# Optimization experiments

Measured on AMD Instinct MI355X. Metric: run time of the kernel, lower is better.

## Reference

```python
import jax, jax.numpy as jnp
import numpy as np
from jax.scipy.special import gammaln

RES = 512    # init res
STEPS = 128  # init steps


def setup_inputs() -> dict:
    key = jax.random.key(0)
    # control points in [0,1]^2: [batch, n_strks, n_points, 2]
    control_points = jax.random.uniform(key, (16, 4, 4, 2), dtype=jnp.float32)
    sigma = jnp.float32(0.02)  # Gaussian kernel bandwidth
    return {"control_points": control_points, "sigma": sigma}


def _bernstein(order, n_steps):
    # feat[k, t] = C(order, k) * t**(order-k) * (1-t)**k, matching sample_curve
    t = jnp.linspace(0.0, 1.0, n_steps, dtype=jnp.float32)          # [T]
    k = jnp.arange(order + 1, dtype=jnp.float32)[:, None]           # [K,1]
    o = jnp.float32(order)
    log_comb = gammaln(o + 1.0) - gammaln(k + 1.0) - gammaln(o - k + 1.0)
    return jnp.exp(log_comb) * t[None, :] ** (o - k) * (1.0 - t[None, :]) ** k  # [K,T]


def reference(control_points, sigma):
    """Bezier.forward with method='base', keep_strk_dim=True.
    Returns [batch, n_strks, 1, res, res]."""
    b, s, n_pts, _ = control_points.shape
    feat = _bernstein(n_pts - 1, STEPS)                              # [K,T]
    curve = jnp.einsum('bcki,kt->bcit', control_points, feat)       # [b,s,2,T]
    x = curve[:, :, 0]                                               # [b,s,T]
    y = curve[:, :, 1]                                               # [b,s,T]
    g = jnp.arange(RES, dtype=jnp.float32) / RES                     # pixel coords
    inv = 1.0 / (2.0 * sigma ** 2)
    # Gaussian splat is separable: exp(-(dx^2+dy^2)/2s^2) = exp(-dx^2/2s^2)*exp(-dy^2/2s^2)
    # raster[b,s,p,q] = sum_t Ay[b,s,t,p] * Ax[b,s,t,q]  (x indexes columns q, y rows p,
    # matching torch meshgrid + transpose(1,3) layout)
    Ax = jnp.exp(-(x[..., None] - g) ** 2 * inv)                     # [b,s,T,res]
    Ay = jnp.exp(-(y[..., None] - g) ** 2 * inv)                     # [b,s,T,res]
    raster = jnp.einsum('bstp,bstq->bspq', Ay, Ax)                   # [b,s,res,res]
    return raster[:, :, None]                                        # [b,s,1,res,res]
```

## Files before the change

kernel.cpp:

```cpp
#include <hip/hip_runtime.h>
#include <math.h>

#define RES    512
#define STEPS  128
#define BH     16
#define NCHUNK 8

__global__ __launch_bounds__(256) void bezier_band_kernel(
    const float* __restrict__ cp,
    const float* __restrict__ sigma_ptr,
    float* __restrict__ out)
{
    __shared__ float xb[STEPS];
    __shared__ float yb[STEPS];
    __shared__ float ayc[STEPS][BH];
    __shared__ unsigned char clist[NCHUNK][STEPS];
    __shared__ int  ccnt[NCHUNK];
    __shared__ int  nb_s;

    const int img  = blockIdx.y;
    const int p0   = blockIdx.x * BH;
    const int tid  = threadIdx.x;
    const int lane = tid & 63;
    const int wave = tid >> 6;

    const float sigma  = sigma_ptr[0];
    const float inv    = 1.0f / (2.0f * sigma * sigma);
    const float msq    = 16.0f / inv;
    const float margin = sqrtf(msq);

    if (tid == 0) nb_s = 0;
    __syncthreads();

    if (tid < STEPS) {
        const float w  = (float)tid * (1.0f / 127.0f);
        const float v  = 1.0f - w;
        const float b0 = w * w * w;
        const float b1 = 3.0f * w * w * v;
        const float b2 = 3.0f * w * v * v;
        const float b3 = v * v * v;
        const float* c = cp + (size_t)img * 8;
        const float x = c[0]*b0 + c[2]*b1 + c[4]*b2 + c[6]*b3;
        const float y = c[1]*b0 + c[3]*b1 + c[5]*b2 + c[7]*b3;
        const float lo = (float)p0            * (1.0f / RES) - margin;
        const float hi = (float)(p0 + BH - 1) * (1.0f / RES) + margin;
        if (y >= lo && y <= hi) {
            const int s = atomicAdd(&nb_s, 1);
            xb[s] = x;
            yb[s] = y;
        }
    }
    __syncthreads();
    const int nb = nb_s;

    for (int e = tid; e < nb * BH; e += 256) {
        const int s = e >> 4;
        const int i = e & (BH - 1);
        const float dy = yb[s] - (float)(p0 + i) * (1.0f / RES);
        ayc[s][i] = __expf(-dy * dy * inv);
    }

    #pragma unroll
    for (int cc = 0; cc < 2; ++cc) {
        const int c = wave + 4 * cc;
        const float lo = (float)(c * 64)      * (1.0f / RES) - margin;
        const float hi = (float)(c * 64 + 63) * (1.0f / RES) + margin;
        int cnt = 0;
        for (int base = 0; base < nb; base += 64) {
            const int s = base + lane;
            const bool act = (s < nb) && (xb[s] >= lo) && (xb[s] <= hi);
            const unsigned long long m = __ballot(act);
            if (act) {
                const int pos = __popcll(m & ((1ull << lane) - 1ull));
                clist[c][cnt + pos] = (unsigned char)s;
            }
            cnt += __popcll(m);
        }
        if (lane == 0) ccnt[c] = cnt;
    }
    __syncthreads();

    float acc0[BH], acc1[BH];
    #pragma unroll
    for (int i = 0; i < BH; ++i) { acc0[i] = 0.0f; acc1[i] = 0.0f; }

    const float gq0 = (float)tid         * (1.0f / RES);
    const float gq1 = (float)(tid + 256) * (1.0f / RES);
    const int c0 = wave;
    const int c1 = wave + 4;

    const int n0 = ccnt[c0];
    for (int j = 0; j < n0; ++j) {
        const int   s  = clist[c0][j];
        const float dx = xb[s] - gq0;
        const float ax = __expf(-dx * dx * inv);
        const float4 a0 = *(const float4*)&ayc[s][0];
        const float4 a1 = *(const float4*)&ayc[s][4];
        const float4 a2 = *(const float4*)&ayc[s][8];
        const float4 a3 = *(const float4*)&ayc[s][12];
        acc0[0]  += ax * a0.x; acc0[1]  += ax * a0.y;
        acc0[2]  += ax * a0.z; acc0[3]  += ax * a0.w;
        acc0[4]  += ax * a1.x; acc0[5]  += ax * a1.y;
        acc0[6]  += ax * a1.z; acc0[7]  += ax * a1.w;
        acc0[8]  += ax * a2.x; acc0[9]  += ax * a2.y;
        acc0[10] += ax * a2.z; acc0[11] += ax * a2.w;
        acc0[12] += ax * a3.x; acc0[13] += ax * a3.y;
        acc0[14] += ax * a3.z; acc0[15] += ax * a3.w;
    }
    const int n1 = ccnt[c1];
    for (int j = 0; j < n1; ++j) {
        const int   s  = clist[c1][j];
        const float dx = xb[s] - gq1;
        const float ax = __expf(-dx * dx * inv);
        const float4 a0 = *(const float4*)&ayc[s][0];
        const float4 a1 = *(const float4*)&ayc[s][4];
        const float4 a2 = *(const float4*)&ayc[s][8];
        const float4 a3 = *(const float4*)&ayc[s][12];
        acc1[0]  += ax * a0.x; acc1[1]  += ax * a0.y;
        acc1[2]  += ax * a0.z; acc1[3]  += ax * a0.w;
        acc1[4]  += ax * a1.x; acc1[5]  += ax * a1.y;
        acc1[6]  += ax * a1.z; acc1[7]  += ax * a1.w;
        acc1[8]  += ax * a2.x; acc1[9]  += ax * a2.y;
        acc1[10] += ax * a2.z; acc1[11] += ax * a2.w;
        acc1[12] += ax * a3.x; acc1[13] += ax * a3.y;
        acc1[14] += ax * a3.z; acc1[15] += ax * a3.w;
    }

    #pragma unroll
    for (int i = 0; i < BH; ++i) {
        const size_t rowoff = ((size_t)img * RES + (size_t)(p0 + i)) * RES;
        out[rowoff + tid]       = acc0[i];
        out[rowoff + tid + 256] = acc1[i];
    }
}

extern "C" void kernel_launch(void* const* d_in, const int* in_sizes, int n_in,
                              void* d_out, int out_size, void* d_ws, size_t ws_size,
                              hipStream_t stream) {
    const float* cp    = (const float*)d_in[0];
    const float* sigma = (const float*)d_in[1];
    float* out         = (float*)d_out;
    const int n_img    = in_sizes[0] / 8;
    dim3 grid(RES / BH, n_img);
    bezier_band_kernel<<<grid, 256, 0, stream>>>(cp, sigma, out);
}
```

Measured before the change: 92.42 us.

## Use 512-thread blocks, one column chunk per wave, with image-interleaved block order

Blocks grow from 256 to 512 threads, so each wave handles a single 64-column chunk with one 16-row accumulator set instead of two sequential chunks. This halves per-thread serial work and register pressure. The grid is flattened with the image index in the low bits so neighbouring blocks cover different images, which spreads load across compute units. The hit loop is also unrolled by two. The hard-coded `& 63` assumes exactly 64 images and breaks for any other batch size.

```diff
diff --git a/kernel.cpp b/kernel.cpp
--- a/kernel.cpp
+++ b/kernel.cpp
@@ -6,7 +6,7 @@
 #define BH     16
 #define NCHUNK 8
 
-__global__ __launch_bounds__(256) void bezier_band_kernel(
+__global__ __launch_bounds__(512) void bezier_band_kernel(
     const float* __restrict__ cp,
     const float* __restrict__ sigma_ptr,
     float* __restrict__ out)
@@ -18,8 +18,9 @@
     __shared__ int  ccnt[NCHUNK];
     __shared__ int  nb_s;
 
-    const int img  = blockIdx.y;
-    const int p0   = blockIdx.x * BH;
+    const int bid  = blockIdx.x;
+    const int img  = bid & 63;
+    const int p0   = (bid >> 6) * BH;
     const int tid  = threadIdx.x;
     const int lane = tid & 63;
     const int wave = tid >> 6;
@@ -53,18 +54,16 @@
     __syncthreads();
     const int nb = nb_s;
 
-    for (int e = tid; e < nb * BH; e += 256) {
+    for (int e = tid; e < nb * BH; e += 512) {
         const int s = e >> 4;
         const int i = e & (BH - 1);
         const float dy = yb[s] - (float)(p0 + i) * (1.0f / RES);
         ayc[s][i] = __expf(-dy * dy * inv);
     }
 
-    #pragma unroll
-    for (int cc = 0; cc < 2; ++cc) {
-        const int c = wave + 4 * cc;
-        const float lo = (float)(c * 64)      * (1.0f / RES) - margin;
-        const float hi = (float)(c * 64 + 63) * (1.0f / RES) + margin;
+    {
+        const float lo = (float)(wave * 64)      * (1.0f / RES) - margin;
+        const float hi = (float)(wave * 64 + 63) * (1.0f / RES) + margin;
         int cnt = 0;
         for (int base = 0; base < nb; base += 64) {
             const int s = base + lane;
@@ -72,65 +71,57 @@
             const unsigned long long m = __ballot(act);
             if (act) {
                 const int pos = __popcll(m & ((1ull << lane) - 1ull));
-                clist[c][cnt + pos] = (unsigned char)s;
+                clist[wave][cnt + pos] = (unsigned char)s;
             }
             cnt += __popcll(m);
         }
-        if (lane == 0) ccnt[c] = cnt;
+        if (lane == 0) ccnt[wave] = cnt;
     }
     __syncthreads();
 
-    float acc0[BH], acc1[BH];
+    float acc[BH];
     #pragma unroll
-    for (int i = 0; i < BH; ++i) { acc0[i] = 0.0f; acc1[i] = 0.0f; }
+    for (int i = 0; i < BH; ++i) acc[i] = 0.0f;
 
-    const float gq0 = (float)tid         * (1.0f / RES);
-    const float gq1 = (float)(tid + 256) * (1.0f / RES);
-    const int c0 = wave;
-    const int c1 = wave + 4;
+    const float gq = (float)tid * (1.0f / RES);
+    const int   n  = ccnt[wave];
+    const unsigned char* __restrict__ cl = clist[wave];
 
-    const int n0 = ccnt[c0];
-    for (int j = 0; j < n0; ++j) {
-        const int   s  = clist[c0][j];
-        const float dx = xb[s] - gq0;
-        const float ax = __expf(-dx * dx * inv);
-        const float4 a0 = *(const float4*)&ayc[s][0];
-        const float4 a1 = *(const float4*)&ayc[s][4];
-        const float4 a2 = *(const float4*)&ayc[s][8];
-        const float4 a3 = *(const float4*)&ayc[s][12];
-        acc0[0]  += ax * a0.x; acc0[1]  += ax * a0.y;
-        acc0[2]  += ax * a0.z; acc0[3]  += ax * a0.w;
-        acc0[4]  += ax * a1.x; acc0[5]  += ax * a1.y;
-        acc0[6]  += ax * a1.z; acc0[7]  += ax * a1.w;
-        acc0[8]  += ax * a2.x; acc0[9]  += ax * a2.y;
-        acc0[10] += ax * a2.z; acc0[11] += ax * a2.w;
-        acc0[12] += ax * a3.x; acc0[13] += ax * a3.y;
-        acc0[14] += ax * a3.z; acc0[15] += ax * a3.w;
+    #define HIT_BODY(S)                                                    \
+        do {                                                               \
+            const float dx = xb[(S)] - gq;                                 \
+            const float ax = __expf(-dx * dx * inv);                       \
+            const float4 a0 = *(const float4*)&ayc[(S)][0];                \
+            const float4 a1 = *(const float4*)&ayc[(S)][4];                \
+            const float4 a2 = *(const float4*)&ayc[(S)][8];                \
+            const float4 a3 = *(const float4*)&ayc[(S)][12];               \
+            acc[0]  += ax * a0.x; acc[1]  += ax * a0.y;                    \
+            acc[2]  += ax * a0.z; acc[3]  += ax * a0.w;                    \
+            acc[4]  += ax * a1.x; acc[5]  += ax * a1.y;                    \
+            acc[6]  += ax * a1.z; acc[7]  += ax * a1.w;                    \
+            acc[8]  += ax * a2.x; acc[9]  += ax * a2.y;                    \
+            acc[10] += ax * a2.z; acc[11] += ax * a2.w;                    \
+            acc[12] += ax * a3.x; acc[13] += ax * a3.y;                    \
+            acc[14] += ax * a3.z; acc[15] += ax * a3.w;                    \
+        } while (0)
+
+    int j = 0;
+    for (; j + 2 <= n; j += 2) {
+        const int s0 = cl[j];
+        const int s1 = cl[j + 1];
+        HIT_BODY(s0);
+        HIT_BODY(s1);
     }
-    const int n1 = ccnt[c1];
-    for (int j = 0; j < n1; ++j) {
-        const int   s  = clist[c1][j];
-        const float dx = xb[s] - gq1;
-        const float ax = __expf(-dx * dx * inv);
-        const float4 a0 = *(const float4*)&ayc[s][0];
-        const float4 a1 = *(const float4*)&ayc[s][4];
-        const float4 a2 = *(const float4*)&ayc[s][8];
-        const float4 a3 = *(const float4*)&ayc[s][12];
-        acc1[0]  += ax * a0.x; acc1[1]  += ax * a0.y;
-        acc1[2]  += ax * a0.z; acc1[3]  += ax * a0.w;
-        acc1[4]  += ax * a1.x; acc1[5]  += ax * a1.y;
-        acc1[6]  += ax * a1.z; acc1[7]  += ax * a1.w;
-        acc1[8]  += ax * a2.x; acc1[9]  += ax * a2.y;
-        acc1[10] += ax * a2.z; acc1[11] += ax * a2.w;
-        acc1[12] += ax * a3.x; acc1[13] += ax * a3.y;
-        acc1[14] += ax * a3.z; acc1[15] += ax * a3.w;
+    if (j < n) {
+        const int s0 = cl[j];
+        HIT_BODY(s0);
     }
+    #undef HIT_BODY
 
     #pragma unroll
     for (int i = 0; i < BH; ++i) {
         const size_t rowoff = ((size_t)img * RES + (size_t)(p0 + i)) * RES;
-        out[rowoff + tid]       = acc0[i];
-        out[rowoff + tid + 256] = acc1[i];
+        out[rowoff + tid] = acc[i];
     }
 }
 
@@ -141,6 +132,6 @@
     const float* sigma = (const float*)d_in[1];
     float* out         = (float*)d_out;
     const int n_img    = in_sizes[0] / 8;
-    dim3 grid(RES / BH, n_img);
-    bezier_band_kernel<<<grid, 256, 0, stream>>>(cp, sigma, out);
+    const int nblocks  = (RES / BH) * n_img;
+    bezier_band_kernel<<<nblocks, 512, 0, stream>>>(cp, sigma, out);
 }
```

After: 91.40 us. Within noise of the previous version (-1.1%).
